# Performance work log

Hardware: AMD Instinct MI355X
Metric: run time of the kernel (lower is better)

Reference implementation:

```python
import jax, jax.numpy as jnp
import numpy as np

B, T, C, H = 1, 4096, 768, 12
D = C // H  # head_dim = 64


def setup_inputs() -> dict:
    key = jax.random.key(0)
    ks = jax.random.split(key, 5)
    s = 1.0 / np.sqrt(C)
    return {
        "x": jax.random.normal(ks[0], (B, T, C), dtype=jnp.float32),
        "Wq": jax.random.normal(ks[1], (C, C), dtype=jnp.float32) * s,
        "bq": jnp.zeros((C,), dtype=jnp.float32),
        "Wk": jax.random.normal(ks[2], (C, C), dtype=jnp.float32) * s,
        "bk": jnp.zeros((C,), dtype=jnp.float32),
        "Wv": jax.random.normal(ks[3], (C, C), dtype=jnp.float32) * s,
        "bv": jnp.zeros((C,), dtype=jnp.float32),
        "Wo": jax.random.normal(ks[4], (C, C), dtype=jnp.float32) * s,
        "bo": jnp.zeros((C,), dtype=jnp.float32),
    }


def reference(x, Wq, bq, Wk, bk, Wv, bv, Wo, bo):
    # Linear projections (torch nn.Linear: y = x @ W.T + b)
    q = (x @ Wq.T + bq).reshape(B, T, H, D).transpose(0, 2, 1, 3)  # [B,H,T,D]
    k = (x @ Wk.T + bk).reshape(B, T, H, D).transpose(0, 2, 1, 3)
    v = (x @ Wv.T + bv).reshape(B, T, H, D).transpose(0, 2, 1, 3)
    scale = 1.0 / jnp.sqrt(jnp.asarray(D, dtype=x.dtype))
    scores = jnp.einsum("bhqd,bhkd->bhqk", q, k) * scale  # [B,H,T,T]
    attn = jax.nn.softmax(scores, axis=-1)
    out = jnp.einsum("bhqk,bhkd->bhqd", attn, v)  # [B,H,T,D]
    y = out.transpose(0, 2, 1, 3).reshape(B, T, C)
    return y @ Wo.T + bo
```

## Files before the change

### kernel.cpp

```cpp
#include <hip/hip_runtime.h>
#include <math.h>

#define T_ 4096
#define C_ 768
#define H_ 12
#define D_ 64
#define TC_ ((size_t)T_ * C_)
#define CC_ ((size_t)C_ * C_)

typedef __attribute__((ext_vector_type(8))) __bf16 bf16x8;
typedef __attribute__((ext_vector_type(4))) __bf16 bf16x4;
typedef __attribute__((ext_vector_type(2))) __bf16 bf16x2;
typedef __attribute__((ext_vector_type(4))) float f32x4;
typedef __attribute__((ext_vector_type(16))) float f32x16;
typedef __attribute__((ext_vector_type(8))) unsigned short u16x8;
typedef __attribute__((ext_vector_type(4))) unsigned int u32x4;

#define MFIX 24.0f

static __device__ __forceinline__ float fast_exp2(float x) {
#if __has_builtin(__builtin_amdgcn_exp2f)
    return __builtin_amdgcn_exp2f(x);
#else
    return exp2f(x);
#endif
}

static __device__ __forceinline__ unsigned pack2(float a, float b) {
    bf16x2 v = { (__bf16)a, (__bf16)b };
    return __builtin_bit_cast(unsigned, v);
}

static __device__ __forceinline__ void gload16(const void* g, void* l) {
    __builtin_amdgcn_global_load_lds(
        (const __attribute__((address_space(1))) unsigned int*)g,
        (__attribute__((address_space(3))) unsigned int*)l, 16, 0, 0);
}

__global__ void f2b_kernel(const float* __restrict__ in,
                           unsigned short* __restrict__ out, int n4) {
    int i = blockIdx.x * blockDim.x + threadIdx.x;
    const int stride = gridDim.x * blockDim.x;
    for (; i < n4; i += stride) {
        float4 v = ((const float4*)in)[i];
        bf16x4 o = { (__bf16)v.x, (__bf16)v.y, (__bf16)v.z, (__bf16)v.w };
        *(bf16x4*)&out[(size_t)i * 4] = o;
    }
}

__global__ void f2b4_kernel(const float* __restrict__ w0, const float* __restrict__ w1,
                            const float* __restrict__ w2, const float* __restrict__ w3,
                            unsigned short* __restrict__ out) {
    const float* src = (blockIdx.y == 0) ? w0 : (blockIdx.y == 1) ? w1
                     : (blockIdx.y == 2) ? w2 : w3;
    unsigned short* dst = out + (size_t)blockIdx.y * CC_;
    const int i = blockIdx.x * blockDim.x + threadIdx.x;
    float4 v = ((const float4*)src)[i];
    bf16x4 o = { (__bf16)v.x, (__bf16)v.y, (__bf16)v.z, (__bf16)v.w };
    *(bf16x4*)&dst[(size_t)i * 4] = o;
}

#define BM 128
#define BN 128
#define BKG 64

struct GemmRegs {
    const unsigned short* ag[4];
    const unsigned short* wg[4];
    unsigned short* la[4];
    unsigned short* lw[4];
    int lq, lg, wr, wc;
};

static __device__ __forceinline__ void gemm_setup(
    GemmRegs& R, const unsigned short* A, const unsigned short* W,
    unsigned short* Asm, unsigned short* Bsm, int bm, int bn, int K)
{
    const int tid = threadIdx.x;
    const int wave = tid >> 6, lane = tid & 63;
    R.lq = lane & 15; R.lg = lane >> 4;
    R.wr = wave >> 1; R.wc = wave & 1;
#pragma unroll
    for (int i = 0; i < 4; ++i) {
        const int flat = wave * 256 + i * 64 + lane;
        const int row = flat >> 3, cb = flat & 7;
        R.ag[i] = A + (size_t)(bm + row) * K + cb * 8;
        R.wg[i] = W + (size_t)(bn + row) * K + cb * 8;
        R.la[i] = Asm + (wave * 4 + i) * 512;
        R.lw[i] = Bsm + (wave * 4 + i) * 512;
    }
}

static __device__ __forceinline__ void gemm_loop(
    GemmRegs& R, unsigned short* Asm, unsigned short* Bsm, int K, f32x4 acc[4][4])
{
    for (int kb = 0; kb < K; kb += BKG) {
        __syncthreads();
#pragma unroll
        for (int i = 0; i < 4; ++i) {
            gload16(R.ag[i] + kb, R.la[i]);
            gload16(R.wg[i] + kb, R.lw[i]);
        }
        __syncthreads();
        __builtin_amdgcn_s_setprio(1);
#pragma unroll
        for (int ks = 0; ks < 2; ++ks) {
            bf16x8 af[4], wf[4];
#pragma unroll
            for (int m = 0; m < 4; ++m)
                af[m] = *(const bf16x8*)&Asm[(R.wr * 64 + m * 16 + R.lq) * BKG + ks * 32 + R.lg * 8];
#pragma unroll
            for (int n = 0; n < 4; ++n)
                wf[n] = *(const bf16x8*)&Bsm[(R.wc * 64 + n * 16 + R.lq) * BKG + ks * 32 + R.lg * 8];
#pragma unroll
            for (int m = 0; m < 4; ++m)
#pragma unroll
                for (int n = 0; n < 4; ++n)
                    acc[m][n] = __builtin_amdgcn_mfma_f32_16x16x32_bf16(af[m], wf[n], acc[m][n], 0, 0, 0);
        }
        __builtin_amdgcn_s_setprio(0);
    }
}

__global__ __launch_bounds__(256) void qkv128(
    const unsigned short* __restrict__ xb,
    const unsigned short* __restrict__ Wqb, const unsigned short* __restrict__ Wkb,
    const unsigned short* __restrict__ Wvb,
    const float* __restrict__ bq, const float* __restrict__ bk, const float* __restrict__ bv,
    unsigned short* __restrict__ Qb, unsigned short* __restrict__ Kb,
    unsigned short* __restrict__ Vtb)
{
    __shared__ unsigned short Asm[BM * BKG];
    __shared__ unsigned short Bsm[BN * BKG];
    const int z = blockIdx.z;
    const unsigned short* W = (z == 0) ? Wqb : (z == 1) ? Wkb : Wvb;
    const float* bias = (z == 0) ? bq : (z == 1) ? bk : bv;
    const int bm = blockIdx.x * BM, bn = blockIdx.y * BN;

    GemmRegs R;
    gemm_setup(R, xb, W, Asm, Bsm, bm, bn, C_);
    f32x4 acc[4][4] = {};
    gemm_loop(R, Asm, Bsm, C_, acc);

    const float sc = (z == 0) ? 0.18033688011112042f : 1.0f;
#pragma unroll
    for (int mt = 0; mt < 4; ++mt) {
        const int m0 = bm + R.wr * 64 + mt * 16 + R.lg * 4;
#pragma unroll
        for (int nt = 0; nt < 4; ++nt) {
            const int n = bn + R.wc * 64 + nt * 16 + R.lq;
            const float b = bias[n];
            if (z == 2) {
                bf16x4 o = { (__bf16)(acc[mt][nt][0] + b), (__bf16)(acc[mt][nt][1] + b),
                             (__bf16)(acc[mt][nt][2] + b), (__bf16)(acc[mt][nt][3] + b) };
                *(bf16x4*)&Vtb[(size_t)n * T_ + m0] = o;
            } else {
                unsigned short* Y = (z == 0) ? Qb : Kb;
#pragma unroll
                for (int r = 0; r < 4; ++r)
                    Y[(size_t)(m0 + r) * C_ + n] =
                        __builtin_bit_cast(unsigned short, (__bf16)((acc[mt][nt][r] + b) * sc));
            }
        }
    }
}

__global__ __launch_bounds__(256) void out128(
    const unsigned short* __restrict__ ctxb, const unsigned short* __restrict__ Wob,
    const float* __restrict__ bo, float* __restrict__ out)
{
    __shared__ unsigned short Asm[BM * BKG];
    __shared__ unsigned short Bsm[BN * BKG];
    const int bm = blockIdx.x * BM, bn = blockIdx.y * BN;

    GemmRegs R;
    gemm_setup(R, ctxb, Wob, Asm, Bsm, bm, bn, C_);
    f32x4 acc[4][4] = {};
    gemm_loop(R, Asm, Bsm, C_, acc);

#pragma unroll
    for (int mt = 0; mt < 4; ++mt) {
        const int m0 = bm + R.wr * 64 + mt * 16 + R.lg * 4;
#pragma unroll
        for (int nt = 0; nt < 4; ++nt) {
            const int n = bn + R.wc * 64 + nt * 16 + R.lq;
            const float b = bo[n];
#pragma unroll
            for (int r = 0; r < 4; ++r)
                out[(size_t)(m0 + r) * C_ + n] = acc[mt][nt][r] + b;
        }
    }
}

template <int SPLITS>
__global__ __launch_bounds__(128, 3) void attn32s(
    const unsigned short* __restrict__ Qb, const unsigned short* __restrict__ Kb,
    const unsigned short* __restrict__ Vtb, unsigned short* __restrict__ Opart,
    float* __restrict__ lpart)
{
    __shared__ unsigned short Ks[64 * 64];
    __shared__ unsigned short Vs[64 * 64];

    const int tid = threadIdx.x;
    const int wave = tid >> 6, lane = tid & 63;
    const int lq = lane & 31, hi = lane >> 5;

    const int perx = (SPLITS * 768) / 8;
    const int bid = blockIdx.x;
    const int sw = (bid & 7) * perx + (bid >> 3);
    const int split = sw / 768;
    const int rem = sw - split * 768;
    const int h = rem >> 6, qt = rem & 63;
    const int q0 = qt * 64 + wave * 32;
    const int kv0 = split * (T_ / SPLITS);
    const int KVTILES = T_ / 64 / SPLITS;

    const int swz = (lq & 7) << 4;
    int rof[4];
#pragma unroll
    for (int ks = 0; ks < 4; ++ks)
        rof[ks] = lq * 128 + ((hi * 16 + ks * 32) ^ swz);

    bf16x8 qf[4];
    {
        const unsigned short* qp = Qb + (size_t)(q0 + lq) * C_ + h * D_ + hi * 8;
#pragma unroll
        for (int ks = 0; ks < 4; ++ks) qf[ks] = *(const bf16x8*)(qp + ks * 16);
    }

    const int srow = (lane >> 3);
    const int soff = (lane & 7) * 16;
    const char* gkb = (const char*)Kb +
        (size_t)(kv0 + wave * 32 + srow) * (C_ * 2) + h * (D_ * 2) + soff;
    const char* gvb = (const char*)Vtb +
        (size_t)(h * D_ + wave * 32 + srow) * (T_ * 2) + kv0 * 2 + soff;
    char* kds = (char*)Ks + (wave * 32 + srow) * 128 + (soff ^ (srow << 4));
    char* vds = (char*)Vs + (wave * 32 + srow) * 128 + (soff ^ (srow << 4));

    u16x8 kreg[4], vreg[4];
#pragma unroll
    for (int k = 0; k < 4; ++k) {
        kreg[k] = *(const u16x8*)(gkb + k * 8 * (C_ * 2));
        vreg[k] = *(const u16x8*)(gvb + k * 8 * (T_ * 2));
    }

    f32x16 oacc0 = {}, oacc1 = {};
    float lrun = 0.f;

    for (int it = 0; it < KVTILES; ++it) {
        __syncthreads();
#pragma unroll
        for (int k = 0; k < 4; ++k) {
            *(u16x8*)(kds + k * 1024) = kreg[k];
            *(u16x8*)(vds + k * 1024) = vreg[k];
        }
        __syncthreads();

        if (it + 1 < KVTILES) {
            const char* gk = gkb + (size_t)(it + 1) * 64 * (C_ * 2);
            const char* gv = gvb + (size_t)(it + 1) * 128;
#pragma unroll
            for (int k = 0; k < 4; ++k) {
                kreg[k] = *(const u16x8*)(gk + k * 8 * (C_ * 2));
                vreg[k] = *(const u16x8*)(gv + k * 8 * (T_ * 2));
            }
        }

        const char* kb = (const char*)&Ks[0];
        const char* vb = (const char*)&Vs[0];

        f32x16 s0 = {}, s1 = {};
        __builtin_amdgcn_s_setprio(1);
#pragma unroll
        for (int ks = 0; ks < 4; ++ks) {
            bf16x8 kf0 = *(const bf16x8*)(kb + rof[ks]);
            bf16x8 kf1 = *(const bf16x8*)(kb + 4096 + rof[ks]);
            s0 = __builtin_amdgcn_mfma_f32_32x32x16_bf16(kf0, qf[ks], s0, 0, 0, 0);
            s1 = __builtin_amdgcn_mfma_f32_32x32x16_bf16(kf1, qf[ks], s1, 0, 0, 0);
        }
        __builtin_amdgcn_s_setprio(0);

#pragma unroll
        for (int r = 0; r < 16; ++r) {
            s0[r] = fast_exp2(s0[r] - MFIX);
            s1[r] = fast_exp2(s1[r] - MFIX);
        }
        {
            float ps[8];
#pragma unroll
            for (int r = 0; r < 8; ++r)
                ps[r] = (s0[r] + s0[r + 8]) + (s1[r] + s1[r + 8]);
            ps[0] += ps[4]; ps[1] += ps[5]; ps[2] += ps[6]; ps[3] += ps[7];
            float pt = (ps[0] + ps[1]) + (ps[2] + ps[3]);
            lrun += pt + __shfl_xor(pt, 32);
        }

        bf16x8 pf[4];
#pragma unroll
        for (int half = 0; half < 2; ++half) {
            const f32x16& s = half ? s1 : s0;
            unsigned g[8];
#pragma unroll
            for (int a = 0; a < 8; ++a) g[a] = pack2(s[2 * a], s[2 * a + 1]);
            unsigned V0 = hi ? g[0] : g[2];
            unsigned V1 = hi ? g[1] : g[3];
            unsigned xV0 = __shfl_xor((int)V0, 32);
            unsigned xV1 = __shfl_xor((int)V1, 32);
            u32x4 pk0 = { hi ? xV0 : g[0], hi ? xV1 : g[1],
                          hi ? g[2] : xV0, hi ? g[3] : xV1 };
            pf[2 * half + 0] = __builtin_bit_cast(bf16x8, pk0);
            unsigned W0 = hi ? g[4] : g[6];
            unsigned W1 = hi ? g[5] : g[7];
            unsigned xW0 = __shfl_xor((int)W0, 32);
            unsigned xW1 = __shfl_xor((int)W1, 32);
            u32x4 pk1 = { hi ? xW0 : g[4], hi ? xW1 : g[5],
                          hi ? g[6] : xW0, hi ? g[7] : xW1 };
            pf[2 * half + 1] = __builtin_bit_cast(bf16x8, pk1);
        }

        __builtin_amdgcn_s_setprio(1);
#pragma unroll
        for (int ks = 0; ks < 4; ++ks) {
            bf16x8 vf0 = *(const bf16x8*)(vb + rof[ks]);
            bf16x8 vf1 = *(const bf16x8*)(vb + 4096 + rof[ks]);
            oacc0 = __builtin_amdgcn_mfma_f32_32x32x16_bf16(vf0, pf[ks], oacc0, 0, 0, 0);
            oacc1 = __builtin_amdgcn_mfma_f32_32x32x16_bf16(vf1, pf[ks], oacc1, 0, 0, 0);
        }
        __builtin_amdgcn_s_setprio(0);
    }

    unsigned short* op = Opart + ((size_t)(split * H_ + h) * T_ + q0 + lq) * 64;
#pragma unroll
    for (int k = 0; k < 4; ++k) {
        bf16x4 o0 = { (__bf16)oacc0[4 * k + 0], (__bf16)oacc0[4 * k + 1],
                      (__bf16)oacc0[4 * k + 2], (__bf16)oacc0[4 * k + 3] };
        *(bf16x4*)&op[8 * k + 4 * hi] = o0;
        bf16x4 o1 = { (__bf16)oacc1[4 * k + 0], (__bf16)oacc1[4 * k + 1],
                      (__bf16)oacc1[4 * k + 2], (__bf16)oacc1[4 * k + 3] };
        *(bf16x4*)&op[32 + 8 * k + 4 * hi] = o1;
    }
    if (hi == 0)
        lpart[(size_t)(split * H_ + h) * T_ + q0 + lq] = lrun;
}

template <int SPLITS>
__global__ __launch_bounds__(256) void combineS(
    const unsigned short* __restrict__ Opart, const float* __restrict__ lpart,
    unsigned short* __restrict__ ctxb)
{
    const int idx = blockIdx.x * 256 + threadIdx.x;
    const int dq = idx & 15;
    const int ht = idx >> 4;
    const int h = ht >> 12;
    const int t = ht & (T_ - 1);

    float denom = 0.f;
#pragma unroll
    for (int sp = 0; sp < SPLITS; ++sp)
        denom += lpart[(size_t)(sp * H_ + h) * T_ + t];
    const float inv = 1.f / denom;

    float acc[4] = {};
#pragma unroll
    for (int sp = 0; sp < SPLITS; ++sp) {
        const bf16x4 a = *(const bf16x4*)&Opart[((size_t)(sp * H_ + h) * T_ + t) * 64 + dq * 4];
#pragma unroll
        for (int i = 0; i < 4; ++i) acc[i] += (float)a[i];
    }
    bf16x4 r;
#pragma unroll
    for (int i = 0; i < 4; ++i) r[i] = (__bf16)(acc[i] * inv);
    *(bf16x4*)&ctxb[(size_t)t * C_ + h * D_ + dq * 4] = r;
}

extern "C" void kernel_launch(void* const* d_in, const int* in_sizes, int n_in,
                              void* d_out, int out_size, void* d_ws, size_t ws_size,
                              hipStream_t stream) {
    (void)in_sizes; (void)n_in; (void)out_size;
    const float* x  = (const float*)d_in[0];
    const float* Wq = (const float*)d_in[1];
    const float* bq = (const float*)d_in[2];
    const float* Wk = (const float*)d_in[3];
    const float* bk = (const float*)d_in[4];
    const float* Wv = (const float*)d_in[5];
    const float* bv = (const float*)d_in[6];
    const float* Wo = (const float*)d_in[7];
    const float* bo = (const float*)d_in[8];
    float* out = (float*)d_out;

    unsigned short* ws    = (unsigned short*)d_ws;
    unsigned short* xb    = ws;
    unsigned short* Wqb   = xb + TC_;
    unsigned short* Wkb   = Wqb + CC_;
    unsigned short* Wvb   = Wkb + CC_;
    unsigned short* Wob   = Wvb + CC_;
    unsigned short* Qb    = Wob + CC_;
    unsigned short* Kb    = Qb + TC_;
    unsigned short* Vtb   = Kb + TC_;
    unsigned short* ctxb  = Vtb + TC_;
    unsigned short* Opart = ctxb + TC_;

    const size_t lsz = (size_t)H_ * T_ * sizeof(float);
    const size_t need4 = (size_t)(9 * TC_ + 4 * CC_) * 2 + 4 * lsz;
    const int S = (ws_size >= need4) ? 4 : 2;

    f2b_kernel<<<2048, 256, 0, stream>>>(x, xb, (int)(TC_ / 4));
    dim3 gw(CC_ / 4 / 256, 4);
    f2b4_kernel<<<gw, 256, 0, stream>>>(Wq, Wk, Wv, Wo, Wqb);

    dim3 gq(T_ / BM, C_ / BN, 3);
    qkv128<<<gq, 256, 0, stream>>>(xb, Wqb, Wkb, Wvb, bq, bk, bv, Qb, Kb, Vtb);

    if (S == 4) {
        float* lpart = (float*)(Opart + 4 * TC_);
        attn32s<4><<<4 * 768, 128, 0, stream>>>(Qb, Kb, Vtb, Opart, lpart);
        combineS<4><<<(T_ * H_ * 16) / 256, 256, 0, stream>>>(Opart, lpart, ctxb);
    } else {
        float* lpart = (float*)(Opart + 2 * TC_);
        attn32s<2><<<2 * 768, 128, 0, stream>>>(Qb, Kb, Vtb, Opart, lpart);
        combineS<2><<<(T_ * H_ * 16) / 256, 256, 0, stream>>>(Opart, lpart, ctxb);
    }

    dim3 go(T_ / BM, C_ / BN);
    out128<<<go, 256, 0, stream>>>(ctxb, Wob, bo, out);
}
```

Before: 144.8 us.

## Use 4-wave attention blocks sharing KV tiles and fix split count to two

The attention kernel now runs 256 threads (4 waves, 128 query rows) per block instead of 2 waves, so each K/V tile staged in LDS serves twice as many queries and each thread loads half as many vectors. The KV split is fixed at 2 rather than 4 when workspace allows, giving 768 larger blocks and a simpler two-way combine. This halves redundant KV global traffic per query, but leaves fewer and longer blocks with less parallelism across the device.

```diff
diff --git a/kernel.cpp b/kernel.cpp
--- a/kernel.cpp
+++ b/kernel.cpp
@@ -192,8 +192,10 @@
     }
 }
 
-template <int SPLITS>
-__global__ __launch_bounds__(128, 3) void attn32s(
+#define SPLITS 2
+#define KVTILES (T_ / 64 / SPLITS)
+
+__global__ __launch_bounds__(256, 3) void attn32s(
     const unsigned short* __restrict__ Qb, const unsigned short* __restrict__ Kb,
     const unsigned short* __restrict__ Vtb, unsigned short* __restrict__ Opart,
     float* __restrict__ lpart)
@@ -205,15 +207,13 @@
     const int wave = tid >> 6, lane = tid & 63;
     const int lq = lane & 31, hi = lane >> 5;
 
-    const int perx = (SPLITS * 768) / 8;
     const int bid = blockIdx.x;
-    const int sw = (bid & 7) * perx + (bid >> 3);
-    const int split = sw / 768;
-    const int rem = sw - split * 768;
-    const int h = rem >> 6, qt = rem & 63;
-    const int q0 = qt * 64 + wave * 32;
+    const int sw = (bid & 7) * 96 + (bid >> 3);
+    const int split = sw / 384;
+    const int rem = sw - split * 384;
+    const int h = rem >> 5, qt = rem & 31;
+    const int q0 = qt * 128 + wave * 32;
     const int kv0 = split * (T_ / SPLITS);
-    const int KVTILES = T_ / 64 / SPLITS;
 
     const int swz = (lq & 7) << 4;
     int rof[4];
@@ -228,20 +228,26 @@
         for (int ks = 0; ks < 4; ++ks) qf[ks] = *(const bf16x8*)(qp + ks * 16);
     }
 
-    const int srow = (lane >> 3);
-    const int soff = (lane & 7) * 16;
-    const char* gkb = (const char*)Kb +
-        (size_t)(kv0 + wave * 32 + srow) * (C_ * 2) + h * (D_ * 2) + soff;
-    const char* gvb = (const char*)Vtb +
-        (size_t)(h * D_ + wave * 32 + srow) * (T_ * 2) + kv0 * 2 + soff;
-    char* kds = (char*)Ks + (wave * 32 + srow) * 128 + (soff ^ (srow << 4));
-    char* vds = (char*)Vs + (wave * 32 + srow) * 128 + (soff ^ (srow << 4));
-
-    u16x8 kreg[4], vreg[4];
-#pragma unroll
-    for (int k = 0; k < 4; ++k) {
-        kreg[k] = *(const u16x8*)(gkb + k * 8 * (C_ * 2));
-        vreg[k] = *(const u16x8*)(gvb + k * 8 * (T_ * 2));
+    const char* gk[2];
+    const char* gv[2];
+    char* kds[2];
+    char* vds[2];
+#pragma unroll
+    for (int j = 0; j < 2; ++j) {
+        const int f = j * 256 + tid;
+        const int row = f >> 3;
+        const int col = (f & 7) * 16;
+        gk[j] = (const char*)Kb + (size_t)(kv0 + row) * (C_ * 2) + h * (D_ * 2) + col;
+        gv[j] = (const char*)Vtb + (size_t)(h * D_ + row) * (T_ * 2) + kv0 * 2 + col;
+        kds[j] = (char*)Ks + row * 128 + (col ^ ((row & 7) << 4));
+        vds[j] = (char*)Vs + row * 128 + (col ^ ((row & 7) << 4));
+    }
+
+    u16x8 kreg[2], vreg[2];
+#pragma unroll
+    for (int j = 0; j < 2; ++j) {
+        kreg[j] = *(const u16x8*)(gk[j]);
+        vreg[j] = *(const u16x8*)(gv[j]);
     }
 
     f32x16 oacc0 = {}, oacc1 = {};
@@ -250,19 +256,19 @@
     for (int it = 0; it < KVTILES; ++it) {
         __syncthreads();
 #pragma unroll
-        for (int k = 0; k < 4; ++k) {
-            *(u16x8*)(kds + k * 1024) = kreg[k];
-            *(u16x8*)(vds + k * 1024) = vreg[k];
+        for (int j = 0; j < 2; ++j) {
+            *(u16x8*)kds[j] = kreg[j];
+            *(u16x8*)vds[j] = vreg[j];
         }
         __syncthreads();
 
         if (it + 1 < KVTILES) {
-            const char* gk = gkb + (size_t)(it + 1) * 64 * (C_ * 2);
-            const char* gv = gvb + (size_t)(it + 1) * 128;
-#pragma unroll
-            for (int k = 0; k < 4; ++k) {
-                kreg[k] = *(const u16x8*)(gk + k * 8 * (C_ * 2));
-                vreg[k] = *(const u16x8*)(gv + k * 8 * (T_ * 2));
+            const size_t ko = (size_t)(it + 1) * 64 * (C_ * 2);
+            const size_t vo = (size_t)(it + 1) * 128;
+#pragma unroll
+            for (int j = 0; j < 2; ++j) {
+                kreg[j] = *(const u16x8*)(gk[j] + ko);
+                vreg[j] = *(const u16x8*)(gv[j] + vo);
             }
         }
 
@@ -343,8 +349,7 @@
         lpart[(size_t)(split * H_ + h) * T_ + q0 + lq] = lrun;
 }
 
-template <int SPLITS>
-__global__ __launch_bounds__(256) void combineS(
+__global__ __launch_bounds__(256) void combine2(
     const unsigned short* __restrict__ Opart, const float* __restrict__ lpart,
     unsigned short* __restrict__ ctxb)
 {
@@ -354,29 +359,22 @@
     const int h = ht >> 12;
     const int t = ht & (T_ - 1);
 
-    float denom = 0.f;
-#pragma unroll
-    for (int sp = 0; sp < SPLITS; ++sp)
-        denom += lpart[(size_t)(sp * H_ + h) * T_ + t];
-    const float inv = 1.f / denom;
-
-    float acc[4] = {};
-#pragma unroll
-    for (int sp = 0; sp < SPLITS; ++sp) {
-        const bf16x4 a = *(const bf16x4*)&Opart[((size_t)(sp * H_ + h) * T_ + t) * 64 + dq * 4];
-#pragma unroll
-        for (int i = 0; i < 4; ++i) acc[i] += (float)a[i];
-    }
+    const float l0 = lpart[(size_t)h * T_ + t];
+    const float l1 = lpart[(size_t)(H_ + h) * T_ + t];
+    const float inv = 1.f / (l0 + l1);
+    const bf16x4 a0 = *(const bf16x4*)&Opart[((size_t)h * T_ + t) * 64 + dq * 4];
+    const bf16x4 a1 = *(const bf16x4*)&Opart[((size_t)(H_ + h) * T_ + t) * 64 + dq * 4];
     bf16x4 r;
 #pragma unroll
-    for (int i = 0; i < 4; ++i) r[i] = (__bf16)(acc[i] * inv);
+    for (int i = 0; i < 4; ++i)
+        r[i] = (__bf16)(((float)a0[i] + (float)a1[i]) * inv);
     *(bf16x4*)&ctxb[(size_t)t * C_ + h * D_ + dq * 4] = r;
 }
 
 extern "C" void kernel_launch(void* const* d_in, const int* in_sizes, int n_in,
                               void* d_out, int out_size, void* d_ws, size_t ws_size,
                               hipStream_t stream) {
-    (void)in_sizes; (void)n_in; (void)out_size;
+    (void)in_sizes; (void)n_in; (void)out_size; (void)ws_size;
     const float* x  = (const float*)d_in[0];
     const float* Wq = (const float*)d_in[1];
     const float* bq = (const float*)d_in[2];
@@ -399,10 +397,7 @@
     unsigned short* Vtb   = Kb + TC_;
     unsigned short* ctxb  = Vtb + TC_;
     unsigned short* Opart = ctxb + TC_;
-
-    const size_t lsz = (size_t)H_ * T_ * sizeof(float);
-    const size_t need4 = (size_t)(9 * TC_ + 4 * CC_) * 2 + 4 * lsz;
-    const int S = (ws_size >= need4) ? 4 : 2;
+    float* lpart = (float*)(Opart + 2 * TC_);
 
     f2b_kernel<<<2048, 256, 0, stream>>>(x, xb, (int)(TC_ / 4));
     dim3 gw(CC_ / 4 / 256, 4);
@@ -411,15 +406,8 @@
     dim3 gq(T_ / BM, C_ / BN, 3);
     qkv128<<<gq, 256, 0, stream>>>(xb, Wqb, Wkb, Wvb, bq, bk, bv, Qb, Kb, Vtb);
 
-    if (S == 4) {
-        float* lpart = (float*)(Opart + 4 * TC_);
-        attn32s<4><<<4 * 768, 128, 0, stream>>>(Qb, Kb, Vtb, Opart, lpart);
-        combineS<4><<<(T_ * H_ * 16) / 256, 256, 0, stream>>>(Opart, lpart, ctxb);
-    } else {
-        float* lpart = (float*)(Opart + 2 * TC_);
-        attn32s<2><<<2 * 768, 128, 0, stream>>>(Qb, Kb, Vtb, Opart, lpart);
-        combineS<2><<<(T_ * H_ * 16) / 256, 256, 0, stream>>>(Opart, lpart, ctxb);
-    }
+    attn32s<<<768, 256, 0, stream>>>(Qb, Kb, Vtb, Opart, lpart);
+    combine2<<<(T_ * H_ * 16) / 256, 256, 0, stream>>>(Opart, lpart, ctxb);
 
     dim3 go(T_ / BM, C_ / BN);
     out128<<<go, 256, 0, stream>>>(ctxb, Wob, bo, out);
```

After: 134.2 us. -7.3%, faster.
